# Kernel optimization log

Measured on AMD Instinct MI355X. Metric: run time of the kernel, lower is better.

## Reference

```python
import jax, jax.numpy as jnp
import numpy as np

SOC, EOS = 3, 2
NUM_HEADS = 12
LN_EPS = 1e-5


def setup_inputs() -> dict:
    key = jax.random.key(0)
    ks = jax.random.split(key, 24)
    B, S, D, N, FF, K = 8, 4096, 768, 1024, 3072, 640
    img = jax.random.normal(ks[0], (B, N, D), jnp.float32)
    hid = jax.random.normal(ks[1], (B, S, D), jnp.float32)
    seq = jax.random.randint(ks[2], (B, S), 4, 100)
    m = jax.random.uniform(ks[3], (B, S)) < 0.125
    seq = jnp.where(m, SOC, seq).at[:, 0].set(SOC)  # ensure >=1 SOC per row
    w = lambda k, a, b: jax.random.normal(k, (a, b), jnp.float32) * 0.02
    return {
        "img": img, "hid": hid, "seq": seq,
        "wq_s": w(ks[4], D, D), "wk_s": w(ks[5], D, D), "wv_s": w(ks[6], D, D), "wo_s": w(ks[7], D, D),
        "wq_c": w(ks[8], D, D), "wk_c": w(ks[9], D, D), "wv_c": w(ks[10], D, D), "wo_c": w(ks[11], D, D),
        "w_ff1": w(ks[12], D, FF), "w_ff2": w(ks[13], FF, D),
        "ln1_s": jnp.ones((D,)), "ln1_b": jnp.zeros((D,)),
        "ln2_s": jnp.ones((D,)), "ln2_b": jnp.zeros((D,)),
        "ln3_s": jnp.ones((D,)), "ln3_b": jnp.zeros((D,)),
        "cap": K,
    }


def _ln(x, s, b):
    mu = jnp.mean(x, axis=-1, keepdims=True)
    var = jnp.var(x, axis=-1, keepdims=True)
    return (x - mu) * jax.lax.rsqrt(var + LN_EPS) * s + b


def _mha(q_in, kv_in, wq, wk, wv, wo, key_mask):
    # q_in [B,Lq,D], kv_in [B,Lk,D], key_mask [B,Lk] bool or None
    B, Lq, D = q_in.shape
    H = NUM_HEADS
    dh = D // H
    q = (q_in @ wq).reshape(B, Lq, H, dh)
    k = (kv_in @ wk).reshape(B, -1, H, dh)
    v = (kv_in @ wv).reshape(B, -1, H, dh)
    scores = jnp.einsum("bqhd,bkhd->bhqk", q, k) / np.sqrt(dh).astype(q.dtype)
    if key_mask is not None:
        scores = jnp.where(key_mask[:, None, None, :], scores, jnp.asarray(-1e9, scores.dtype))
    att = jax.nn.softmax(scores, axis=-1)
    out = jnp.einsum("bhqk,bkhd->bqhd", att, v).reshape(B, Lq, D)
    return out @ wo


def _extract(data, mask, cap):
    # data [B,S,...], mask [B,S] bool -> packed+zero-padded [B,cap,...]
    pos = jnp.cumsum(mask, axis=1) - 1          # slot for each valid token
    pos = jnp.where(mask, pos, cap)             # invalid tokens -> dump slot
    def one(d, p):
        buf = jnp.zeros((cap + 1,) + d.shape[1:], d.dtype)
        return buf.at[p].set(d)[:cap]
        # note: dump slot cap is sliced away
    return jax.vmap(one)(data, pos), pos


def reference(img, hid, seq, wq_s, wk_s, wv_s, wo_s, wq_c, wk_c, wv_c, wo_c,
              w_ff1, w_ff2, ln1_s, ln1_b, ln2_s, ln2_b, ln3_s, ln3_b, cap):
    # mask: SOC tokens occurring before the first EOS
    soc = (seq == SOC) & (jnp.cumsum(seq == EOS, axis=1) == 0)  # [B,S]
    ext, pos = _extract(hid, soc, cap)                          # [B,K,D]
    counts = jnp.sum(soc, axis=1)                               # [B]
    run = jnp.arange(cap)[None, :] < counts[:, None]            # [B,K] valid slots

    # Blocks: pre-LN self-attn (key mask = run), cross-attn to img, FFN
    x = ext
    x = x + _mha(_ln(x, ln1_s, ln1_b), _ln(x, ln1_s, ln1_b), wq_s, wk_s, wv_s, wo_s, run)
    x = x + _mha(_ln(x, ln2_s, ln2_b), img, wq_c, wk_c, wv_c, wo_c, None)
    h = _ln(x, ln3_s, ln3_b)
    x = x + jax.nn.gelu(h @ w_ff1) @ w_ff2

    # masked_scatter back: each SOC position (b,s) takes x[b, pos[b,s]]
    idx = jnp.clip(pos, 0, cap - 1)
    gathered = jnp.take_along_axis(x, idx[:, :, None], axis=1)  # [B,S,D]
    hid_new = jnp.where(soc[:, :, None], gathered, hid)
    return hid_new, x
```

## Files before the change

kernel.cpp:

```cpp
#include <hip/hip_runtime.h>
#include <hip/hip_bf16.h>


#define B_    8
#define S_    4096
#define D_    768
#define N_    1024
#define FF_   3072
#define H_    12
#define DH_   64
#define KCAP  640
#define SOC_TOK 3
#define EOS_TOK 2

typedef __hip_bfloat16 bf16;
typedef unsigned short u16;
typedef __attribute__((ext_vector_type(8))) short short8;
typedef __attribute__((ext_vector_type(4))) float f32x4;

__device__ __forceinline__ u16 ftou16(float x){ union{bf16 b; u16 s;} c; c.b = __float2bfloat16(x); return c.s; }
__device__ __forceinline__ unsigned pk2(float lo, float hi){ return (unsigned)ftou16(lo) | ((unsigned)ftou16(hi)<<16); }

__device__ __forceinline__ f32x4 MFMA(short8 a, short8 b, f32x4 c){
  return __builtin_amdgcn_mfma_f32_16x16x32_bf16(a, b, c, 0, 0, 0);
}

__device__ __forceinline__ void gld16(const void* gp, void* lp){
  __builtin_amdgcn_global_load_lds(
    reinterpret_cast<const __attribute__((address_space(1))) unsigned int*>((size_t)gp),
    reinterpret_cast<__attribute__((address_space(3))) unsigned int*>((size_t)lp),
    16, 0, 0);
}

template<int N> __device__ __forceinline__ void vwait(){
  asm volatile("s_waitcnt vmcnt(%0)" :: "i"(N) : "memory");
}
__device__ __forceinline__ void wgbar(){ asm volatile("s_barrier" ::: "memory"); }

__device__ __forceinline__ int xcd_swz(){
  int id = blockIdx.x;
  return (id & 7) * ((int)gridDim.x >> 3) + (id >> 3);
}

__device__ void scan_body(const int* __restrict__ seq, int* __restrict__ pos,
                          int* __restrict__ src, int* __restrict__ counts, int b){
  int tid = threadIdx.x;
  __shared__ int sd[256];
  __shared__ int carryE, carryS;
  if (tid==0){ carryE=0; carryS=0; }
  __syncthreads();
  for (int c=0; c<S_; c+=256){
    int s   = c + tid;
    int tok = seq[b*S_ + s];
    int isE = (tok==EOS_TOK) ? 1 : 0;
    int isS = (tok==SOC_TOK) ? 1 : 0;
    sd[tid]=isE; __syncthreads();
    for (int off=1; off<256; off<<=1){ int t_=(tid>=off)?sd[tid-off]:0; __syncthreads(); sd[tid]+=t_; __syncthreads(); }
    int eIncl = sd[tid];
    int eTot  = sd[255];
    int valid = (isS && (carryE + eIncl)==0) ? 1 : 0;
    __syncthreads();
    sd[tid]=valid; __syncthreads();
    for (int off=1; off<256; off<<=1){ int t_=(tid>=off)?sd[tid-off]:0; __syncthreads(); sd[tid]+=t_; __syncthreads(); }
    int vIncl = sd[tid];
    int vTot  = sd[255];
    if (valid){
      int slot = carryS + vIncl - 1;
      pos[b*S_ + s] = slot;
      if (slot < KCAP) src[b*KCAP + slot] = s;
    } else {
      pos[b*S_ + s] = -1;
    }
    __syncthreads();
    if (tid==0){ carryE += eTot; carryS += vTot; }
    __syncthreads();
  }
  if (tid==0) counts[b] = (carryS < KCAP) ? carryS : KCAP;
}

struct TransArgs { const float* w[10]; u16* o[10]; };
__global__ __launch_bounds__(256) void transpose_scan_k(TransArgs a, const int* __restrict__ seq,
                                                        int* __restrict__ pos, int* __restrict__ src,
                                                        int* __restrict__ counts,
                                                        const float* __restrict__ img, u16* __restrict__ imgB){
  int id = blockIdx.x;
  if (id >= 9224){
    int base = (id - 9224)*2048 + threadIdx.x*8;
    float4 a0 = *(const float4*)(img + base);
    float4 a1 = *(const float4*)(img + base + 4);
    uint4 wv;
    wv.x = pk2(a0.x,a0.y); wv.y = pk2(a0.z,a0.w); wv.z = pk2(a1.x,a1.y); wv.w = pk2(a1.z,a1.w);
    *(uint4*)(imgB + base) = wv;
    return;
  }
  if (id >= 9216){ scan_body(seq, pos, src, counts, id - 9216); return; }
  __shared__ float tile[32][33];
  int wi, t, K, N;
  if (id < 4608){ wi = id/576; t = id%576; K = 768; N = 768; }
  else if (id < 6912){ wi = 8; t = id-4608; K = 768; N = 3072; }
  else { wi = 9; t = id-6912; K = 3072; N = 768; }
  const float* in = a.w[wi]; u16* out = a.o[wi];
  int nbx = N >> 5;
  int bx = t % nbx, by = t / nbx;
  int tx = threadIdx.x & 31, ty = threadIdx.x >> 5;
  #pragma unroll
  for (int i=0;i<4;++i)
    tile[ty + i*8][tx] = in[(size_t)(by*32 + ty + i*8)*N + bx*32 + tx];
  __syncthreads();
  #pragma unroll
  for (int i=0;i<4;++i)
    out[(size_t)(bx*32 + ty + i*8)*K + by*32 + tx] = ftou16(tile[tx][ty + i*8]);
}

__global__ __launch_bounds__(256) void prep_k(const float* __restrict__ hid,
                                              const int* __restrict__ src,
                                              const int* __restrict__ counts,
                                              const int* __restrict__ pos,
                                              const float* __restrict__ g, const float* __restrict__ bt,
                                              float* __restrict__ X, u16* __restrict__ T0,
                                              float* __restrict__ out0){
  int id = blockIdx.x; int tid = threadIdx.x;
  if (id >= 5120){
    int base = (id - 5120)*4;
    #pragma unroll
    for (int r2=0;r2<4;++r2){
      int bs = base + r2;
      if (pos[bs] >= 0) continue;
      const float* hr = hid + (size_t)bs*D_;
      float* orow = out0 + (size_t)bs*D_;
      orow[tid]     = hr[tid];
      orow[tid+256] = hr[tid+256];
      orow[tid+512] = hr[tid+512];
    }
    return;
  }
  int bk = id; int b = bk / KCAP; int k = bk % KCAP;
  float v0, v1, v2;
  if (k < counts[b]){
    const float* hr = hid + ((size_t)b*S_ + src[b*KCAP + k])*D_;
    v0 = hr[tid]; v1 = hr[tid+256]; v2 = hr[tid+512];
  } else { v0 = v1 = v2 = 0.f; }
  float* xr = X + (size_t)bk*D_;
  xr[tid] = v0; xr[tid+256] = v1; xr[tid+512] = v2;
  float s1=v0+v1+v2, s2=v0*v0+v1*v1+v2*v2;
  for (int off=32; off; off>>=1){ s1+=__shfl_xor(s1,off); s2+=__shfl_xor(s2,off); }
  __shared__ float red[8];
  __shared__ float mu_s, rs_s;
  int w=tid>>6, ln=tid&63;
  if (ln==0){ red[w]=s1; red[4+w]=s2; }
  __syncthreads();
  if (tid==0){
    float S1=red[0]+red[1]+red[2]+red[3];
    float S2=red[4]+red[5]+red[6]+red[7];
    float mu = S1*(1.f/D_);
    float var= S2*(1.f/D_) - mu*mu;
    mu_s=mu; rs_s=rsqrtf(var + 1e-5f);
  }
  __syncthreads();
  float mu=mu_s, rs=rs_s;
  u16* yr = T0 + (size_t)bk*D_;
  yr[tid]     = ftou16((v0-mu)*rs*g[tid]     + bt[tid]);
  yr[tid+256] = ftou16((v1-mu)*rs*g[tid+256] + bt[tid+256]);
  yr[tid+512] = ftou16((v2-mu)*rs*g[tid+512] + bt[tid+512]);
}

__global__ __launch_bounds__(256) void ln_k(const float* __restrict__ X, u16* __restrict__ Y,
                                            const float* __restrict__ g, const float* __restrict__ bt){
  int r = blockIdx.x; int tid = threadIdx.x;
  const float* xr = X + (size_t)r*D_;
  float v0=xr[tid], v1=xr[tid+256], v2=xr[tid+512];
  float s1=v0+v1+v2, s2=v0*v0+v1*v1+v2*v2;
  for (int off=32; off; off>>=1){ s1+=__shfl_xor(s1,off); s2+=__shfl_xor(s2,off); }
  __shared__ float red[8];
  __shared__ float mu_s, rs_s;
  int w=tid>>6, ln=tid&63;
  if (ln==0){ red[w]=s1; red[4+w]=s2; }
  __syncthreads();
  if (tid==0){
    float S1=red[0]+red[1]+red[2]+red[3];
    float S2=red[4]+red[5]+red[6]+red[7];
    float mu = S1*(1.f/D_);
    float var= S2*(1.f/D_) - mu*mu;
    mu_s=mu; rs_s=rsqrtf(var + 1e-5f);
  }
  __syncthreads();
  float mu=mu_s, rs=rs_s;
  u16* yr = Y + (size_t)r*D_;
  yr[tid]     = ftou16((v0-mu)*rs*g[tid]     + bt[tid]);
  yr[tid+256] = ftou16((v1-mu)*rs*g[tid+256] + bt[tid+256]);
  yr[tid+512] = ftou16((v2-mu)*rs*g[tid+512] + bt[tid+512]);
}

template<int MODE, int BM, typename TA>
__device__ __forceinline__ void gemm_body(char* ldsp, const TA* __restrict__ A, const u16* __restrict__ Bt,
                                          void* __restrict__ C0, void* __restrict__ C1, void* __restrict__ C2,
                                          int wgid, int N, int K){
  constexpr int MI   = BM/32;
  constexpr int NBUF = (BM==128) ? 2 : ((sizeof(TA)==4) ? 2 : 3);
  u16* As = (u16*)ldsp;
  u16* Bs = (u16*)(ldsp + NBUF*(BM*32)*2);
  int nbx = N >> 7;
  int bx = wgid % nbx, by = wgid / nbx;
  int tid = threadIdx.x;
  int w = tid>>6, l = tid&63, g = l>>4, c = l&15;
  int wr = w&1, wc = w>>1;
  f32x4 acc[MI][4] = {};
  float4 rg[4];
  const int NK = K/32;

  auto STAGEB = [&](int buf, int kt){
    #pragma unroll
    for (int p=0;p<2;++p){
      int row = w*32 + p*16 + (l>>2);
      int su  = (l&3) ^ ((row>>1)&3);
      gld16((const void*)(Bt + (size_t)(bx*128+row)*K + kt + su*8), (void*)&Bs[buf*128*32 + (w*32+p*16)*32]);
    }
  };
  auto STAGEA16 = [&](int buf, int kt){
    if constexpr (BM==128){
      #pragma unroll
      for (int p=0;p<2;++p){
        int row = w*32 + p*16 + (l>>2);
        int su  = (l&3) ^ ((row>>1)&3);
        gld16((const void*)((const u16*)A + (size_t)(by*BM+row)*K + kt + su*8), (void*)&As[buf*BM*32 + (w*32+p*16)*32]);
      }
    } else {
      int row = w*16 + (l>>2);
      int su  = (l&3) ^ ((row>>1)&3);
      gld16((const void*)((const u16*)A + (size_t)(by*BM+row)*K + kt + su*8), (void*)&As[buf*BM*32 + (w*16)*32]);
    }
  };
  auto LOADREG = [&](int kt){
    if constexpr (BM==128){
      const float* ap = (const float*)A + (size_t)(by*BM + (tid>>1))*K + kt + (tid&1)*16;
      rg[0]=*(const float4*)ap;     rg[1]=*(const float4*)(ap+4);
      rg[2]=*(const float4*)(ap+8); rg[3]=*(const float4*)(ap+12);
    } else {
      const float* ap = (const float*)A + (size_t)(by*BM + (tid>>2))*K + kt + (tid&3)*8;
      rg[0] = *(const float4*)ap; rg[1] = *(const float4*)(ap+4);
    }
  };
  auto WRITEA = [&](int buf){
    if constexpr (BM==128){
      int row = tid>>1, half = tid&1;
      uint4 w0,w1;
      w0.x=pk2(rg[0].x,rg[0].y); w0.y=pk2(rg[0].z,rg[0].w); w0.z=pk2(rg[1].x,rg[1].y); w0.w=pk2(rg[1].z,rg[1].w);
      w1.x=pk2(rg[2].x,rg[2].y); w1.y=pk2(rg[2].z,rg[2].w); w1.z=pk2(rg[3].x,rg[3].y); w1.w=pk2(rg[3].z,rg[3].w);
      int sw = (row>>1)&3;
      *(uint4*)&As[buf*BM*32 + row*32 + ((half*2  )^sw)*8] = w0;
      *(uint4*)&As[buf*BM*32 + row*32 + ((half*2+1)^sw)*8] = w1;
    } else {
      int row = tid>>2, unit = tid&3;
      uint4 wv;
      wv.x=pk2(rg[0].x,rg[0].y); wv.y=pk2(rg[0].z,rg[0].w); wv.z=pk2(rg[1].x,rg[1].y); wv.w=pk2(rg[1].z,rg[1].w);
      int sw = (row>>1)&3;
      *(uint4*)&As[buf*BM*32 + row*32 + (unit^sw)*8] = wv;
    }
  };
  auto COMPUTE = [&](int buf){
    short8 af[MI], bfr[4];
    #pragma unroll
    for (int mi=0;mi<MI;++mi){ int row = wr*(MI*16) + mi*16 + c; af[mi]  = *(const short8*)&As[buf*BM*32 + row*32 + (g^((row>>1)&3))*8]; }
    #pragma unroll
    for (int ni=0;ni<4;++ni){ int row = wc*64 + ni*16 + c;       bfr[ni] = *(const short8*)&Bs[buf*128*32 + row*32 + (g^((row>>1)&3))*8]; }
    #pragma unroll
    for (int mi=0;mi<MI;++mi)
      #pragma unroll
      for (int ni=0;ni<4;++ni) acc[mi][ni] = MFMA(af[mi], bfr[ni], acc[mi][ni]);
  };

  if constexpr (BM==128 || sizeof(TA)==4){
    if constexpr (sizeof(TA)==4){ LOADREG(0); STAGEB(0,0); WRITEA(0); }
    else { STAGEA16(0,0); STAGEB(0,0); }
    __syncthreads();
    int buf = 0;
    for (int t=0;t<NK;++t){
      int ktn = (t+1)*32;
      if constexpr (sizeof(TA)==4){
        if (t+1<NK){ LOADREG(ktn); STAGEB(buf^1, ktn); }
        COMPUTE(buf);
        if (t+1<NK) WRITEA(buf^1);
      } else {
        if (t+1<NK){ STAGEA16(buf^1, ktn); STAGEB(buf^1, ktn); }
        COMPUTE(buf);
      }
      __syncthreads();
      buf ^= 1;
    }
  } else {
    constexpr int LPS = 3;
    STAGEA16(0,0);  STAGEB(0,0);
    STAGEA16(1,32); STAGEB(1,32);
    vwait<LPS>();
    wgbar();
    int buf = 0;
    for (int t=0;t<NK;++t){
      if (t+2 < NK){
        int nb = buf+2; if (nb>=3) nb-=3;
        STAGEA16(nb,(t+2)*32); STAGEB(nb,(t+2)*32);
      }
      COMPUTE(buf);
      if (t < NK-2) vwait<LPS>(); else vwait<0>();
      wgbar();
      ++buf; if (buf==3) buf=0;
    }
  }

  int row0 = by*BM + wr*(MI*16), col0 = bx*128 + wc*64;
  #pragma unroll
  for (int mi=0;mi<MI;++mi)
    #pragma unroll
    for (int ni=0;ni<4;++ni){
      int rowb = row0 + mi*16 + g*4;
      int col  = col0 + ni*16 + c;
      if (MODE==4 && col >= 1536){
        int vv = col - 1536; int bb = rowb / KCAP; int key = rowb - bb*KCAP;
        ushort4 pk;
        pk.x = ftou16(acc[mi][ni][0]); pk.y = ftou16(acc[mi][ni][1]);
        pk.z = ftou16(acc[mi][ni][2]); pk.w = ftou16(acc[mi][ni][3]);
        *(ushort4*)&((u16*)C2)[((size_t)(bb*768 + vv))*KCAP + key] = pk;
      } else if (MODE==5 && col >= 768){
        int vv = col - 768; int bb = rowb >> 10; int key = rowb & 1023;
        ushort4 pk;
        pk.x = ftou16(acc[mi][ni][0]); pk.y = ftou16(acc[mi][ni][1]);
        pk.z = ftou16(acc[mi][ni][2]); pk.w = ftou16(acc[mi][ni][3]);
        *(ushort4*)&((u16*)C2)[((size_t)(bb*768 + vv))*1024 + key] = pk;
      } else {
        #pragma unroll
        for (int r=0;r<4;++r){
          int row = rowb + r;
          float v = acc[mi][ni][r];
          if (MODE==0){
            ((u16*)C0)[(size_t)row*N + col] = ftou16(v);
          } else if (MODE==1){
            ((float*)C0)[(size_t)row*N + col] += v;
          } else if (MODE==2){
            float z2 = 1.5957691216057308f*(v + 0.044715f*v*v*v);
            float e  = __expf(z2);
            float th = 1.f - 2.f/(e + 1.f);
            ((u16*)C0)[(size_t)row*N + col] = ftou16(0.5f*v*(1.f+th));
          } else if (MODE==6){
            size_t idx = (size_t)row*N + col;
            ((float*)C1)[idx] = ((const float*)C0)[idx] + v;
          } else if (MODE==4){
            if (col < 768)  ((u16*)C0)[(size_t)row*768 + col]       = ftou16(v);
            else            ((u16*)C1)[(size_t)row*768 + col - 768] = ftou16(v);
          } else {
            ((u16*)C0)[(size_t)row*768 + col] = ftou16(v);
          }
        }
      }
    }
}

template<int MODE, int BM, typename TA>
__global__ __launch_bounds__(256) void gemm_k(const TA* __restrict__ A, const u16* __restrict__ Bt,
                                              void* __restrict__ C0, void* __restrict__ C1, void* __restrict__ C2,
                                              int N, int K){
  constexpr int NBUF = (BM==128) ? 2 : ((sizeof(TA)==4) ? 2 : 3);
  __shared__ __align__(16) char pool[NBUF*(BM+128)*32*2];
  gemm_body<MODE,BM,TA>(pool, A, Bt, C0, C1, C2, xcd_swz(), N, K);
}

__global__ __launch_bounds__(256) void mega1_k(const u16* __restrict__ T0, const u16* __restrict__ wqkv_st,
                                               u16* __restrict__ Qb, u16* __restrict__ Kb, u16* __restrict__ VtS,
                                               const u16* __restrict__ imgB, const u16* __restrict__ wkv_ct,
                                               u16* __restrict__ KbC, u16* __restrict__ VtC){
  __shared__ __align__(16) char pool[2*(128+128)*32*2];
  int wgid = xcd_swz();
  if (wgid < 720) gemm_body<4,128,u16>(pool, T0,   wqkv_st, Qb,  Kb,      VtS, wgid,     2304, 768);
  else            gemm_body<5,128,u16>(pool, imgB, wkv_ct,  KbC, nullptr, VtC, wgid-720, 1536, 768);
}

template<int MASKED>
__global__ __launch_bounds__(256) void attn_k(const u16* __restrict__ Q, const u16* __restrict__ Kb,
                                              const u16* __restrict__ Vt, u16* __restrict__ O,
                                              const int* __restrict__ counts, int Lk){
  __shared__ __align__(16) u16 Ks[3][64*64];
  __shared__ __align__(16) u16 Vs[3][64*64];
  __shared__ __align__(16) u16 P[4][16][72];
  int tid = threadIdx.x;
  int w = tid>>6, l = tid&63, g = l>>4, c = l&15;
  int wgid = xcd_swz();
  int qc = wgid % 5;
  int bh = wgid / 5;
  int h = bh % H_, b = bh / H_;
  int q0 = qc*128 + w*32;
  int cnt = MASKED ? counts[b] : Lk;
  int nt = (cnt + 63) >> 6;

  short8 qf[2][2];
  #pragma unroll
  for (int mi=0;mi<2;++mi){
    const u16* Qrow = Q + ((size_t)(b*KCAP + q0 + mi*16 + c))*D_ + h*DH_;
    qf[mi][0] = *(const short8*)(Qrow + g*8);
    qf[mi][1] = *(const short8*)(Qrow + 32 + g*8);
  }

  int srow8 = (l>>3);
  int sunit = l&7;
  auto STAGE = [&](int buf, int kb){
    #pragma unroll
    for (int p=0;p<2;++p){
      int r0 = w*16 + p*8;
      int rowK = r0 + srow8;
      int su = sunit ^ (rowK&7);
      gld16((const void*)(Kb + ((size_t)(b*Lk + kb + rowK))*D_ + h*DH_ + su*8), (void*)&Ks[buf][r0*64]);
      gld16((const void*)(Vt + ((size_t)(b*D_ + h*DH_ + rowK))*Lk + kb + su*8), (void*)&Vs[buf][r0*64]);
    }
  };

  f32x4 o[2][4] = {};
  float m_[2][4], l_[2][4] = {};
  #pragma unroll
  for (int mi=0;mi<2;++mi)
    #pragma unroll
    for (int r=0;r<4;++r) m_[mi][r] = -1e30f;

  STAGE(0, 0);
  if (nt > 1){ STAGE(1, 64); vwait<4>(); } else { vwait<0>(); }
  wgbar();
  int buf = 0;
  for (int t=0; t<nt; ++t){
    int kb = t*64;
    if (t+2 < nt){
      int nb = buf+2; if (nb>=3) nb-=3;
      STAGE(nb, kb+128);
    }
    short8 fr[4][2];
    #pragma unroll
    for (int nb=0;nb<4;++nb)
      #pragma unroll
      for (int kh=0;kh<2;++kh)
        fr[nb][kh] = *(const short8*)&Ks[buf][(nb*16+c)*64 + (((kh<<2)|g) ^ (c&7))*8];
    f32x4 z[2][4];
    #pragma unroll
    for (int mi=0;mi<2;++mi)
      #pragma unroll
      for (int nb=0;nb<4;++nb){
        f32x4 zz = {0.f,0.f,0.f,0.f};
        zz = MFMA(qf[mi][0], fr[nb][0], zz);
        zz = MFMA(qf[mi][1], fr[nb][1], zz);
        z[mi][nb] = zz;
      }
    float pv[2][4][4];
    #pragma unroll
    for (int nb=0;nb<4;++nb){
      bool msk = MASKED && (kb + nb*16 + c >= cnt);
      #pragma unroll
      for (int mi=0;mi<2;++mi)
        #pragma unroll
        for (int r=0;r<4;++r) pv[mi][nb][r] = msk ? -1e30f : z[mi][nb][r]*0.125f;
    }
    float scl[2][4];
    #pragma unroll
    for (int mi=0;mi<2;++mi){
      #pragma unroll
      for (int r=0;r<4;++r){
        float v = fmaxf(fmaxf(pv[mi][0][r],pv[mi][1][r]), fmaxf(pv[mi][2][r],pv[mi][3][r]));
        v = fmaxf(v, __shfl_xor(v,1)); v = fmaxf(v, __shfl_xor(v,2));
        v = fmaxf(v, __shfl_xor(v,4)); v = fmaxf(v, __shfl_xor(v,8));
        float nm = fmaxf(m_[mi][r], v);
        scl[mi][r] = __expf(m_[mi][r] - nm);
        m_[mi][r] = nm;
      }
      #pragma unroll
      for (int r=0;r<4;++r){
        float acc2 = 0.f;
        #pragma unroll
        for (int nb=0;nb<4;++nb){
          float e = __expf(pv[mi][nb][r] - m_[mi][r]);
          pv[mi][nb][r] = e; acc2 += e;
        }
        acc2 += __shfl_xor(acc2,1); acc2 += __shfl_xor(acc2,2);
        acc2 += __shfl_xor(acc2,4); acc2 += __shfl_xor(acc2,8);
        l_[mi][r] = l_[mi][r]*scl[mi][r] + acc2;
      }
      #pragma unroll
      for (int nbd=0;nbd<4;++nbd)
        #pragma unroll
        for (int r=0;r<4;++r) o[mi][nbd][r] *= scl[mi][r];
    }
    short8 fv[4][2];
    #pragma unroll
    for (int nbd=0;nbd<4;++nbd)
      #pragma unroll
      for (int kh=0;kh<2;++kh)
        fv[nbd][kh] = *(const short8*)&Vs[buf][(nbd*16+c)*64 + (((kh<<2)|g) ^ (c&7))*8];
    #pragma unroll
    for (int mi=0;mi<2;++mi){
      #pragma unroll
      for (int nb=0;nb<4;++nb)
        #pragma unroll
        for (int r=0;r<4;++r) P[w][g*4+r][nb*16+c] = ftou16(pv[mi][nb][r]);
      short8 pa0 = *(const short8*)&P[w][c][g*8];
      short8 pa1 = *(const short8*)&P[w][c][32 + g*8];
      #pragma unroll
      for (int nbd=0;nbd<4;++nbd){
        o[mi][nbd] = MFMA(pa0, fv[nbd][0], o[mi][nbd]);
        o[mi][nbd] = MFMA(pa1, fv[nbd][1], o[mi][nbd]);
      }
    }
    if (t < nt-2) vwait<4>(); else vwait<0>();
    wgbar();
    ++buf; if (buf==3) buf=0;
  }
  #pragma unroll
  for (int mi=0;mi<2;++mi)
    #pragma unroll
    for (int nbd=0;nbd<4;++nbd)
      #pragma unroll
      for (int r=0;r<4;++r)
        O[((size_t)(b*KCAP + q0 + mi*16 + g*4 + r))*D_ + h*DH_ + nbd*16 + c] = ftou16(o[mi][nbd][r] / l_[mi][r]);
}

__global__ __launch_bounds__(256) void scatter_soc_k(const int* __restrict__ pos,
                                                     const float* __restrict__ out1,
                                                     float* __restrict__ out0){
  int base = blockIdx.x*4; int tid = threadIdx.x;
  #pragma unroll
  for (int r2=0;r2<4;++r2){
    int bs = base + r2;
    int p = pos[bs];
    if (p < 0) continue;
    int pc = p < KCAP ? p : (KCAP-1);
    int b = bs >> 12;
    const float* xr = out1 + ((size_t)(b*KCAP + pc))*D_;
    float* orow = out0 + (size_t)bs*D_;
    orow[tid]     = xr[tid];
    orow[tid+256] = xr[tid+256];
    orow[tid+512] = xr[tid+512];
  }
}

extern "C" void kernel_launch(void* const* d_in, const int* in_sizes, int n_in,
                              void* d_out, int out_size, void* d_ws, size_t ws_size,
                              hipStream_t stream){
  const float* img  = (const float*)d_in[0];
  const float* hid  = (const float*)d_in[1];
  const int*   seq  = (const int*)  d_in[2];
  const float* W[10] = { (const float*)d_in[3], (const float*)d_in[4], (const float*)d_in[5], (const float*)d_in[6],
                         (const float*)d_in[7], (const float*)d_in[8], (const float*)d_in[9], (const float*)d_in[10],
                         (const float*)d_in[11], (const float*)d_in[12] };
  const float* ln1s = (const float*)d_in[13];
  const float* ln1b = (const float*)d_in[14];
  const float* ln2s = (const float*)d_in[15];
  const float* ln2b = (const float*)d_in[16];
  const float* ln3s = (const float*)d_in[17];
  const float* ln3b = (const float*)d_in[18];

  char* ws = (char*)d_ws;
  int*   pos    = (int*)  (ws + 0);
  int*   src    = (int*)  (ws + 131072);
  int*   counts = (int*)  (ws + 151552);
  float* X      = (float*)(ws + 151808);
  u16*   T0     = (u16*)  (ws + 15880448);
  u16*   Qb     = (u16*)  (ws + 23744768);
  u16*   Kb     = (u16*)  (ws + 31609088);
  u16*   VtS    = (u16*)  (ws + 39473408);
  u16*   KbC    = (u16*)  (ws + 47337728);
  u16*   VtC    = (u16*)  (ws + 59920640);
  u16*   AO     = (u16*)  (ws + 72503552);
  u16*   Wt     = (u16*)  (ws + 80367872);
  u16*   MID    = Qb;

  u16* wqkv_st = Wt + 0ull*589824;
  u16* wo_st   = Wt + 3ull*589824;
  u16* wq_ct   = Wt + 4ull*589824;
  u16* wkv_ct  = Wt + 5ull*589824;
  u16* wo_ct   = Wt + 7ull*589824;
  u16* wff1t   = Wt + 8ull*589824;
  u16* wff2t   = wff1t + 2359296;

  float* out0 = (float*)d_out;
  float* out1 = out0 + (size_t)B_*S_*D_;
  u16* imgB = (u16*)out1;

  TransArgs ta;
  for (int i=0;i<10;++i) ta.w[i] = W[i];
  for (int i=0;i<8;++i)  ta.o[i] = Wt + (size_t)i*589824;
  ta.o[8] = wff1t; ta.o[9] = wff2t;

  transpose_scan_k<<<12296, 256, 0, stream>>>(ta, seq, pos, src, counts, img, imgB);
  prep_k<<<13312, 256, 0, stream>>>(hid, src, counts, pos, ln1s, ln1b, X, T0, out0);

  const int G_MEGA1 = 720 + 768;
  const int G_N768  = (5120/64)*(768/128);
  const int G_FF1   = (5120/128)*(3072/128);
  const int G_ATT   = B_*H_*5;

  mega1_k<<<G_MEGA1, 256, 0, stream>>>(T0, wqkv_st, Qb, Kb, VtS, imgB, wkv_ct, KbC, VtC);
  attn_k<1><<<G_ATT, 256, 0, stream>>>(Qb, Kb, VtS, AO, counts, KCAP);
  gemm_k<1,64,u16><<<G_N768, 256, 0, stream>>>(AO, wo_st, X, nullptr, nullptr, 768, 768);

  ln_k<<<5120, 256, 0, stream>>>(X, T0, ln2s, ln2b);
  gemm_k<0,64,u16><<<G_N768, 256, 0, stream>>>(T0, wq_ct, Qb, nullptr, nullptr, 768, 768);
  attn_k<0><<<G_ATT, 256, 0, stream>>>(Qb, KbC, VtC, AO, counts, N_);
  gemm_k<1,64,u16><<<G_N768, 256, 0, stream>>>(AO, wo_ct, X, nullptr, nullptr, 768, 768);

  ln_k<<<5120, 256, 0, stream>>>(X, T0, ln3s, ln3b);
  gemm_k<2,128,u16><<<G_FF1, 256, 0, stream>>>(T0, wff1t, MID, nullptr, nullptr, 3072, 768);
  gemm_k<6,64,u16><<<G_N768, 256, 0, stream>>>(MID, wff2t, X, out1, nullptr, 768, 3072);

  scatter_soc_k<<<8192, 256, 0, stream>>>(pos, out1, out0);
}
```

Baseline: 413.3 us.

## Use exp2 with lazy max rescaling and deferred row-sum reduction in attention

Rewrites the attention softmax inner loop to use base-2 exponentials with the log2e factor folded into the score scale. The running max and output rescaling are only updated when any lane's tile max exceeds the old max by a threshold, which skips the per-tile rescale work. The per-lane partial row sums are accumulated locally and cross-lane reduced once at the end instead of every tile. The final division becomes a multiply by a reciprocal. This trades some numerical headroom (values up to 2^11.5 before rescale) for fewer exp, shuffle and multiply instructions per tile.

```diff
diff --git a/kernel.cpp b/kernel.cpp
--- a/kernel.cpp
+++ b/kernel.cpp
@@ -36,6 +36,8 @@
   asm volatile("s_waitcnt vmcnt(%0)" :: "i"(N) : "memory");
 }
 __device__ __forceinline__ void wgbar(){ asm volatile("s_barrier" ::: "memory"); }
+
+__device__ __forceinline__ float fexp2(float x){ float r; asm("v_exp_f32 %0, %1" : "=v"(r) : "v"(x)); return r; }
 
 __device__ __forceinline__ int xcd_swz(){
   int id = blockIdx.x;
@@ -376,6 +378,8 @@
 __global__ __launch_bounds__(256) void attn_k(const u16* __restrict__ Q, const u16* __restrict__ Kb,
                                               const u16* __restrict__ Vt, u16* __restrict__ O,
                                               const int* __restrict__ counts, int Lk){
+  constexpr float C2E  = 0.18033688011112043f;
+  constexpr float THR2 = 11.541560327111707f;
   __shared__ __align__(16) u16 Ks[3][64*64];
   __shared__ __align__(16) u16 Vs[3][64*64];
   __shared__ __align__(16) u16 P[4][16][72];
@@ -411,7 +415,7 @@
   };
 
   f32x4 o[2][4] = {};
-  float m_[2][4], l_[2][4] = {};
+  float m_[2][4], lp[2][4] = {};
   #pragma unroll
   for (int mi=0;mi<2;++mi)
     #pragma unroll
@@ -433,7 +437,7 @@
       #pragma unroll
       for (int kh=0;kh<2;++kh)
         fr[nb][kh] = *(const short8*)&Ks[buf][(nb*16+c)*64 + (((kh<<2)|g) ^ (c&7))*8];
-    f32x4 z[2][4];
+    float pv[2][4][4];
     #pragma unroll
     for (int mi=0;mi<2;++mi)
       #pragma unroll
@@ -441,46 +445,47 @@
         f32x4 zz = {0.f,0.f,0.f,0.f};
         zz = MFMA(qf[mi][0], fr[nb][0], zz);
         zz = MFMA(qf[mi][1], fr[nb][1], zz);
-        z[mi][nb] = zz;
-      }
-    float pv[2][4][4];
-    #pragma unroll
-    for (int nb=0;nb<4;++nb){
-      bool msk = MASKED && (kb + nb*16 + c >= cnt);
-      #pragma unroll
-      for (int mi=0;mi<2;++mi)
+        bool msk = MASKED && (kb + nb*16 + c >= cnt);
         #pragma unroll
-        for (int r=0;r<4;++r) pv[mi][nb][r] = msk ? -1e30f : z[mi][nb][r]*0.125f;
-    }
-    float scl[2][4];
-    #pragma unroll
-    for (int mi=0;mi<2;++mi){
+        for (int r=0;r<4;++r) pv[mi][nb][r] = msk ? -1e30f : zz[r]*C2E;
+      }
+    float tm[2][4];
+    bool need = false;
+    #pragma unroll
+    for (int mi=0;mi<2;++mi)
       #pragma unroll
       for (int r=0;r<4;++r){
         float v = fmaxf(fmaxf(pv[mi][0][r],pv[mi][1][r]), fmaxf(pv[mi][2][r],pv[mi][3][r]));
         v = fmaxf(v, __shfl_xor(v,1)); v = fmaxf(v, __shfl_xor(v,2));
         v = fmaxf(v, __shfl_xor(v,4)); v = fmaxf(v, __shfl_xor(v,8));
-        float nm = fmaxf(m_[mi][r], v);
-        scl[mi][r] = __expf(m_[mi][r] - nm);
-        m_[mi][r] = nm;
-      }
+        tm[mi][r] = v;
+        need = need || (v > m_[mi][r] + THR2);
+      }
+    if (__any(need)){
+      #pragma unroll
+      for (int mi=0;mi<2;++mi)
+        #pragma unroll
+        for (int r=0;r<4;++r){
+          float nm = fmaxf(m_[mi][r], tm[mi][r]);
+          float scl = fexp2(m_[mi][r] - nm);
+          m_[mi][r] = nm;
+          lp[mi][r] *= scl;
+          #pragma unroll
+          for (int nbd=0;nbd<4;++nbd) o[mi][nbd][r] *= scl;
+        }
+    }
+    #pragma unroll
+    for (int mi=0;mi<2;++mi)
       #pragma unroll
       for (int r=0;r<4;++r){
-        float acc2 = 0.f;
+        float acc2 = lp[mi][r];
         #pragma unroll
         for (int nb=0;nb<4;++nb){
-          float e = __expf(pv[mi][nb][r] - m_[mi][r]);
+          float e = fexp2(pv[mi][nb][r] - m_[mi][r]);
           pv[mi][nb][r] = e; acc2 += e;
         }
-        acc2 += __shfl_xor(acc2,1); acc2 += __shfl_xor(acc2,2);
-        acc2 += __shfl_xor(acc2,4); acc2 += __shfl_xor(acc2,8);
-        l_[mi][r] = l_[mi][r]*scl[mi][r] + acc2;
-      }
-      #pragma unroll
-      for (int nbd=0;nbd<4;++nbd)
-        #pragma unroll
-        for (int r=0;r<4;++r) o[mi][nbd][r] *= scl[mi][r];
-    }
+        lp[mi][r] = acc2;
+      }
     short8 fv[4][2];
     #pragma unroll
     for (int nbd=0;nbd<4;++nbd)
@@ -505,13 +510,23 @@
     wgbar();
     ++buf; if (buf==3) buf=0;
   }
+  float linv[2][4];
   #pragma unroll
   for (int mi=0;mi<2;++mi)
     #pragma unroll
+    for (int r=0;r<4;++r){
+      float lf = lp[mi][r];
+      lf += __shfl_xor(lf,1); lf += __shfl_xor(lf,2);
+      lf += __shfl_xor(lf,4); lf += __shfl_xor(lf,8);
+      linv[mi][r] = 1.f/lf;
+    }
+  #pragma unroll
+  for (int mi=0;mi<2;++mi)
+    #pragma unroll
     for (int nbd=0;nbd<4;++nbd)
       #pragma unroll
       for (int r=0;r<4;++r)
-        O[((size_t)(b*KCAP + q0 + mi*16 + g*4 + r))*D_ + h*DH_ + nbd*16 + c] = ftou16(o[mi][nbd][r] / l_[mi][r]);
+        O[((size_t)(b*KCAP + q0 + mi*16 + g*4 + r))*D_ + h*DH_ + nbd*16 + c] = ftou16(o[mi][nbd][r] * linv[mi][r]);
 }
 
 __global__ __launch_bounds__(256) void scatter_soc_k(const int* __restrict__ pos,
```

New measurement: 392.4 us. 5.1% less time.
